# Performance work log

Hardware: AMD Instinct MI355X
Metric: run time of the kernel (lower is better)

## Reference

```python
import jax, jax.numpy as jnp
import numpy as np


def setup_inputs() -> dict:
    key = jax.random.key(0)
    B, D, C, H = 4096, 64, 128, 512
    ks = jax.random.split(key, 6)
    return {
        "q_z_x_params": jax.random.normal(ks[0], (B, C), jnp.float32),
        "eps": jax.random.normal(ks[1], (B, D), jnp.float32),
        "W1": jax.random.normal(ks[2], (D + C, H), jnp.float32) / np.sqrt(D + C).astype(np.float32),
        "b1": jnp.zeros((H,), jnp.float32),
        "W2": jax.random.normal(ks[3], (H, H), jnp.float32) / np.sqrt(H).astype(np.float32),
        "b2": jnp.zeros((H,), jnp.float32),
        "W3": jax.random.normal(ks[4], (H, 2 * D), jnp.float32) / np.sqrt(H).astype(np.float32),
        "b3": jnp.zeros((2 * D,), jnp.float32),
    }


def _made_masks(D, C, H):
    # Standard MADE degrees, natural ordering; context columns fully connected.
    m_in = np.arange(1, D + 1)                      # input degrees 1..D
    m_h = (np.arange(H) % (D - 1)) + 1              # hidden degrees 1..D-1
    M1 = np.concatenate([m_h[None, :] >= m_in[:, None],
                         np.ones((C, H), bool)], axis=0)   # (D+C, H)
    M2 = m_h[None, :] >= m_h[:, None]               # (H, H)
    m_out = np.tile(np.arange(1, D + 1), 2)         # (2D,) mean||prescale
    M3 = m_out[None, :] > m_h[:, None]              # (H, 2D)
    f32 = jnp.float32
    return jnp.asarray(M1, f32), jnp.asarray(M2, f32), jnp.asarray(M3, f32)


def reference(q_z_x_params, eps, W1, b1, W2, b2, W3, b3):
    B, D = eps.shape
    C = q_z_x_params.shape[1]
    H = W2.shape[0]
    M1, M2, M3 = _made_masks(D, C, H)
    mW1, mW2, mW3 = W1 * M1, W2 * M2, W3 * M3

    def made(z):
        x = jnp.concatenate([z, q_z_x_params], axis=1)   # (B, D+C)
        h1 = jax.nn.relu(x @ mW1 + b1)
        h2 = jax.nn.relu(h1 @ mW2 + b2)
        out = h2 @ mW3 + b3                              # (B, 2D)
        return out[:, :D], out[:, D:]

    def step(z, i):
        mean, prescale = made(z)
        mu_i = jnp.take(mean, i, axis=1)                 # (B,)
        scale_i = jax.nn.softplus(jnp.take(prescale, i, axis=1))
        z_i = mu_i + scale_i * jnp.take(eps, i, axis=1)  # reparameterized Normal sample
        z = z.at[:, i].set(z_i)
        return z, None

    z0 = jnp.zeros((B, D), eps.dtype)
    z_sample, _ = jax.lax.scan(step, z0, jnp.arange(D))
    return z_sample
```

## Files before the change

kernel.cpp:

```cpp
#include <hip/hip_runtime.h>
#include <math.h>

#define DD 64
#define CC 128
#define HH 512
#define BATCH 4096

typedef __attribute__((ext_vector_type(2))) float f32x2;

__device__ __forceinline__ f32x2 splat2(float x) { f32x2 v; v[0] = x; v[1] = x; return v; }

__device__ __forceinline__ float fast_softplus(float x) {
    float t = exp2f(-fabsf(x) * 1.44269504f);
    return fmaxf(x, 0.f) + 0.69314718f * log2f(1.f + t);
}

__device__ __forceinline__ float bcast(float x, int l) {
    return __int_as_float(__builtin_amdgcn_readlane(__float_as_int(x), l));
}

typedef const __attribute__((address_space(1))) void* as1_cptr;
typedef __attribute__((address_space(3))) void* as3_ptr;
__device__ __forceinline__ void glds16(const float* g, float* l) {
    __builtin_amdgcn_global_load_lds((as1_cptr)g, (as3_ptr)l, 16, 0, 0);
}

__global__ __launch_bounds__(256, 2) void made_sample(
    const float* __restrict__ ctx,
    const float* __restrict__ eps,
    const float* __restrict__ W1,
    const float* __restrict__ b1,
    const float* __restrict__ W2,
    const float* __restrict__ b2,
    const float* __restrict__ W3,
    const float* __restrict__ b3,
    float* __restrict__ out)
{
    const int lane  = threadIdx.x & 63;
    const int w     = threadIdx.x >> 6;
    const int rbase = blockIdx.x * 8 + w * 2;
    const int jbase = 8 * lane;

    __shared__ float sbuf[2][10 * HH];

    int deg[8];
    #pragma unroll
    for (int u = 0; u < 8; ++u) deg[u] = (jbase + u) % 63 + 1;

    auto load8v = [&](const float* base_, f32x2* r_) {
        float4 a = *(const float4*)(base_ + lane * 4);
        float4 b = *(const float4*)(base_ + 256 + lane * 4);
        r_[0][0] = a.x; r_[0][1] = a.y; r_[1][0] = a.z; r_[1][1] = a.w;
        r_[2][0] = b.x; r_[2][1] = b.y; r_[3][0] = b.z; r_[3][1] = b.w;
    };
    auto stage_row = [&](const float* src, float* dst) {
        glds16(src + lane * 8,     dst);
        glds16(src + lane * 8 + 4, dst + 256);
    };

    f32x2 p1[2][4], p2[2][4], acc[2];
    #pragma unroll
    for (int j = 0; j < 4; ++j) {
        f32x2 t1, t2;
        t1[0] = b1[jbase + 2 * j]; t1[1] = b1[jbase + 2 * j + 1];
        t2[0] = b2[jbase + 2 * j]; t2[1] = b2[jbase + 2 * j + 1];
        p1[0][j] = t1; p1[1][j] = t1;
        p2[0][j] = t2; p2[1][j] = t2;
    }
    acc[0] = splat2(0.f);
    acc[1] = splat2(0.f);

    float ca[2], cb[2], ep[2];
    #pragma unroll
    for (int r = 0; r < 2; ++r) {
        ca[r] = ctx[(rbase + r) * CC + lane];
        cb[r] = ctx[(rbase + r) * CC + 64 + lane];
        ep[r] = eps[(rbase + r) * DD + lane];
    }
    const float b3m = b3[lane];
    const float b3p = b3[64 + lane];

    auto stage_ctx = [&](int ch, float* buf) {
        #pragma unroll
        for (int q2 = 0; q2 < 2; ++q2) {
            const int q = 2 * w + q2;
            stage_row(W1 + (DD + 8 * ch + q) * HH, buf + q * HH);
        }
    };
    auto stage_step = [&](int in, float* buf) {
        const int basen = (in == 0) ? 0 : (in - 1);
        #pragma unroll
        for (int rr = 0; rr < 3; ++rr) {
            const int r = w + 4 * rr;
            if (r <= 9) {
                const float* src;
                if (r < 9) {
                    int k = basen + 63 * r;
                    if (k >= HH) k = HH - 8;
                    src = W2 + k * HH;
                } else {
                    src = W1 + in * HH;
                }
                stage_row(src, buf + r * HH);
            }
        }
    };

    stage_ctx(0, sbuf[0]);
    __syncthreads();
    #pragma unroll 1
    for (int ch = 0; ch < 16; ++ch) {
        float* cur = sbuf[ch & 1];
        float* nxt = sbuf[(ch + 1) & 1];
        if (ch < 15) stage_ctx(ch + 1, nxt);
        else         stage_step(0, sbuf[0]);
        #pragma unroll
        for (int q = 0; q < 8; ++q) {
            f32x2 wv[4];
            load8v(cur + q * HH, wv);
            const int c = 8 * ch + q;
            #pragma unroll
            for (int r = 0; r < 2; ++r) {
                const float cv = bcast((ch < 8) ? ca[r] : cb[r], c & 63);
                const f32x2 cv2 = splat2(cv);
                #pragma unroll
                for (int j = 0; j < 4; ++j) p1[r][j] += cv2 * wv[j];
            }
        }
        __syncthreads();
    }

    float z[2] = {0.f, 0.f};

    #pragma unroll 1
    for (int i = 0; i < DD; ++i) {
        float* cur = sbuf[i & 1];
        float* nxt = sbuf[(i + 1) & 1];
        if (i < 63) stage_step(i + 1, nxt);

        const int base = (i == 0) ? 0 : (i - 1);

        f32x2 w3v[9];
        #pragma unroll
        for (int t = 0; t < 9; ++t) {
            const int k  = base + 63 * t;
            const int ks = (k < HH) ? k : (HH - 1);
            w3v[t][0] = W3[ks * (2 * DD) + lane];
            w3v[t][1] = W3[ks * (2 * DD) + 64 + lane];
        }

        float m[2];
        #pragma unroll
        for (int r = 0; r < 2; ++r) {
            float mv = 0.f;
            #pragma unroll
            for (int u = 0; u < 8; ++u)
                mv = (deg[u] == i) ? p1[r][u >> 1][u & 1] : mv;
            m[r] = fmaxf(mv, 0.f);
        }

        #pragma unroll
        for (int t = 0; t < 9; ++t) {
            const int k = base + 63 * t;
            f32x2 wv[4];
            load8v(cur + t * HH, wv);
            float h0, h1v;
            if (t == 8) {
                const float vm = (k < HH) ? 1.f : 0.f;
                h0  = vm * bcast(m[0], 63);
                h1v = vm * bcast(m[1], 63);
            } else {
                h0  = bcast(m[0], k >> 3);
                h1v = bcast(m[1], k >> 3);
            }
            const f32x2 h0v = splat2(h0), h1vv = splat2(h1v);
            #pragma unroll
            for (int j = 0; j < 4; ++j) {
                p2[0][j] += h0v  * wv[j];
                p2[1][j] += h1vv * wv[j];
            }
        }

        float hn[2];
        #pragma unroll
        for (int r = 0; r < 2; ++r) {
            float hv = 0.f;
            #pragma unroll
            for (int u = 0; u < 8; ++u)
                hv = (deg[u] == i) ? p2[r][u >> 1][u & 1] : hv;
            hn[r] = fmaxf(hv, 0.f);
        }

        #pragma unroll
        for (int t = 0; t < 9; ++t) {
            const int k = base + 63 * t;
            float h0, h1v;
            if (t == 8) {
                const float vm = (k < HH) ? 1.f : 0.f;
                h0  = vm * bcast(hn[0], 63);
                h1v = vm * bcast(hn[1], 63);
            } else {
                h0  = bcast(hn[0], k >> 3);
                h1v = bcast(hn[1], k >> 3);
            }
            acc[0] += splat2(h0)  * w3v[t];
            acc[1] += splat2(h1v) * w3v[t];
        }

        f32x2 w1v[4];
        load8v(cur + 9 * HH, w1v);
        #pragma unroll
        for (int r = 0; r < 2; ++r) {
            const float am = acc[r][0] + b3m;
            const float ap = acc[r][1] + b3p;
            const float sp = fast_softplus(ap);
            const float zc = fmaf(sp, ep[r], am);
            const float zi = bcast(zc, i);
            if (lane == i) z[r] = zi;
            const f32x2 zi2 = splat2(zi);
            #pragma unroll
            for (int j = 0; j < 4; ++j) p1[r][j] += zi2 * w1v[j];
        }

        __syncthreads();
    }

    #pragma unroll
    for (int r = 0; r < 2; ++r) out[(rbase + r) * DD + lane] = z[r];
}

extern "C" void kernel_launch(void* const* d_in, const int* in_sizes, int n_in,
                              void* d_out, int out_size, void* d_ws, size_t ws_size,
                              hipStream_t stream) {
    const float* ctx = (const float*)d_in[0];
    const float* eps = (const float*)d_in[1];
    const float* W1  = (const float*)d_in[2];
    const float* b1  = (const float*)d_in[3];
    const float* W2  = (const float*)d_in[4];
    const float* b2  = (const float*)d_in[5];
    const float* W3  = (const float*)d_in[6];
    const float* b3  = (const float*)d_in[7];
    (void)d_ws; (void)ws_size; (void)in_sizes; (void)n_in; (void)out_size;

    made_sample<<<BATCH / 8, 256, 0, stream>>>(ctx, eps, W1, b1, W2, b2, W3, b3,
                                               (float*)d_out);
}
```

Baseline: 184.7 us.

## Stage W2 and context weights as fp16 and shrink blocks to 128 threads

Adds a pre-kernel that converts W2 and the context rows of W1 to fp16 in the workspace. The main kernel now stages half-width rows into LDS, halving staging traffic and LDS footprint. It also cuts blocks to two waves (4 rows each), doubling the grid. Packed f32x2 FMAs are replaced by scalar fmaf with fp16-to-fp32 converts, and W2 fragments are preloaded into registers. Weight precision drops to fp16, and the extra kernel adds launch overhead.

After: 208.4 us. +12.8%, slower.

```diff
diff --git a/kernel.cpp b/kernel.cpp
--- a/kernel.cpp
+++ b/kernel.cpp
@@ -6,9 +6,14 @@
 #define HH 512
 #define BATCH 4096
 
-typedef __attribute__((ext_vector_type(2))) float f32x2;
-
-__device__ __forceinline__ f32x2 splat2(float x) { f32x2 v; v[0] = x; v[1] = x; return v; }
+typedef _Float16 f16;
+
+__global__ void to_f16(const float* __restrict__ W1, const float* __restrict__ W2,
+                       f16* __restrict__ w2h, f16* __restrict__ w1ch) {
+    int idx = blockIdx.x * 256 + threadIdx.x;
+    if (idx < HH * HH) w2h[idx] = (f16)W2[idx];
+    else               w1ch[idx - HH * HH] = (f16)W1[DD * HH + (idx - HH * HH)];
+}
 
 __device__ __forceinline__ float fast_softplus(float x) {
     float t = exp2f(-fabsf(x) * 1.44269504f);
@@ -21,54 +26,46 @@
 
 typedef const __attribute__((address_space(1))) void* as1_cptr;
 typedef __attribute__((address_space(3))) void* as3_ptr;
-__device__ __forceinline__ void glds16(const float* g, float* l) {
+__device__ __forceinline__ void glds16(const void* g, float* l) {
     __builtin_amdgcn_global_load_lds((as1_cptr)g, (as3_ptr)l, 16, 0, 0);
 }
 
-__global__ __launch_bounds__(256, 2) void made_sample(
+union HW { float4 f4; f16 h[8]; };
+
+#define SLOT_W1 (9 * 256)
+#define BUF_F   (SLOT_W1 + 512)
+
+__global__ __launch_bounds__(128, 2) void made_sample(
     const float* __restrict__ ctx,
     const float* __restrict__ eps,
     const float* __restrict__ W1,
     const float* __restrict__ b1,
-    const float* __restrict__ W2,
     const float* __restrict__ b2,
     const float* __restrict__ W3,
     const float* __restrict__ b3,
+    const f16*   __restrict__ w2h,
+    const f16*   __restrict__ w1ch,
     float* __restrict__ out)
 {
     const int lane  = threadIdx.x & 63;
     const int w     = threadIdx.x >> 6;
-    const int rbase = blockIdx.x * 8 + w * 2;
+    const int rbase = blockIdx.x * 4 + w * 2;
     const int jbase = 8 * lane;
 
-    __shared__ float sbuf[2][10 * HH];
+    __shared__ float sbuf[2][BUF_F];
 
     int deg[8];
     #pragma unroll
     for (int u = 0; u < 8; ++u) deg[u] = (jbase + u) % 63 + 1;
 
-    auto load8v = [&](const float* base_, f32x2* r_) {
-        float4 a = *(const float4*)(base_ + lane * 4);
-        float4 b = *(const float4*)(base_ + 256 + lane * 4);
-        r_[0][0] = a.x; r_[0][1] = a.y; r_[1][0] = a.z; r_[1][1] = a.w;
-        r_[2][0] = b.x; r_[2][1] = b.y; r_[3][0] = b.z; r_[3][1] = b.w;
-    };
-    auto stage_row = [&](const float* src, float* dst) {
-        glds16(src + lane * 8,     dst);
-        glds16(src + lane * 8 + 4, dst + 256);
-    };
-
-    f32x2 p1[2][4], p2[2][4], acc[2];
-    #pragma unroll
-    for (int j = 0; j < 4; ++j) {
-        f32x2 t1, t2;
-        t1[0] = b1[jbase + 2 * j]; t1[1] = b1[jbase + 2 * j + 1];
-        t2[0] = b2[jbase + 2 * j]; t2[1] = b2[jbase + 2 * j + 1];
-        p1[0][j] = t1; p1[1][j] = t1;
-        p2[0][j] = t2; p2[1][j] = t2;
-    }
-    acc[0] = splat2(0.f);
-    acc[1] = splat2(0.f);
+    float p1[2][8], p2[2][8], acc[2][2];
+    #pragma unroll
+    for (int u = 0; u < 8; ++u) {
+        float t1 = b1[jbase + u], t2 = b2[jbase + u];
+        p1[0][u] = t1; p1[1][u] = t1;
+        p2[0][u] = t2; p2[1][u] = t2;
+    }
+    acc[0][0] = 0.f; acc[0][1] = 0.f; acc[1][0] = 0.f; acc[1][1] = 0.f;
 
     float ca[2], cb[2], ep[2];
     #pragma unroll
@@ -82,26 +79,21 @@
 
     auto stage_ctx = [&](int ch, float* buf) {
         #pragma unroll
-        for (int q2 = 0; q2 < 2; ++q2) {
-            const int q = 2 * w + q2;
-            stage_row(W1 + (DD + 8 * ch + q) * HH, buf + q * HH);
-        }
+        for (int q = 0; q < 8; q += 2)
+            glds16(w1ch + (8 * ch + q + w) * HH + lane * 8, buf + (q + w) * 256);
     };
     auto stage_step = [&](int in, float* buf) {
         const int basen = (in == 0) ? 0 : (in - 1);
         #pragma unroll
-        for (int rr = 0; rr < 3; ++rr) {
-            const int r = w + 4 * rr;
-            if (r <= 9) {
-                const float* src;
-                if (r < 9) {
-                    int k = basen + 63 * r;
-                    if (k >= HH) k = HH - 8;
-                    src = W2 + k * HH;
-                } else {
-                    src = W1 + in * HH;
-                }
-                stage_row(src, buf + r * HH);
+        for (int o = w; o < 11; o += 2) {
+            if (o < 9) {
+                int k = basen + 63 * o;
+                if (k >= HH) k = HH - 1;
+                glds16(w2h + k * HH + lane * 8, buf + o * 256);
+            } else if (o == 9) {
+                glds16(W1 + in * HH + lane * 8, buf + SLOT_W1);
+            } else {
+                glds16(W1 + in * HH + lane * 8 + 4, buf + SLOT_W1 + 256);
             }
         }
     };
@@ -116,15 +108,14 @@
         else         stage_step(0, sbuf[0]);
         #pragma unroll
         for (int q = 0; q < 8; ++q) {
-            f32x2 wv[4];
-            load8v(cur + q * HH, wv);
+            HW uw; uw.f4 = *(const float4*)(cur + q * 256 + lane * 4);
             const int c = 8 * ch + q;
             #pragma unroll
             for (int r = 0; r < 2; ++r) {
                 const float cv = bcast((ch < 8) ? ca[r] : cb[r], c & 63);
-                const f32x2 cv2 = splat2(cv);
                 #pragma unroll
-                for (int j = 0; j < 4; ++j) p1[r][j] += cv2 * wv[j];
+                for (int u = 0; u < 8; ++u)
+                    p1[r][u] = fmaf((float)uw.h[u], cv, p1[r][u]);
             }
         }
         __syncthreads();
@@ -140,13 +131,25 @@
 
         const int base = (i == 0) ? 0 : (i - 1);
 
-        f32x2 w3v[9];
+        float w3m[9], w3p[9];
         #pragma unroll
         for (int t = 0; t < 9; ++t) {
             const int k  = base + 63 * t;
             const int ks = (k < HH) ? k : (HH - 1);
-            w3v[t][0] = W3[ks * (2 * DD) + lane];
-            w3v[t][1] = W3[ks * (2 * DD) + 64 + lane];
+            w3m[t] = W3[ks * (2 * DD) + lane];
+            w3p[t] = W3[ks * (2 * DD) + 64 + lane];
+        }
+
+        HW w2v[9];
+        #pragma unroll
+        for (int t = 0; t < 9; ++t)
+            w2v[t].f4 = *(const float4*)(cur + t * 256 + lane * 4);
+        float w1v[8];
+        {
+            float4 a = *(const float4*)(cur + SLOT_W1 + lane * 4);
+            float4 b = *(const float4*)(cur + SLOT_W1 + 256 + lane * 4);
+            w1v[0] = a.x; w1v[1] = a.y; w1v[2] = a.z; w1v[3] = a.w;
+            w1v[4] = b.x; w1v[5] = b.y; w1v[6] = b.z; w1v[7] = b.w;
         }
 
         float m[2];
@@ -154,16 +157,13 @@
         for (int r = 0; r < 2; ++r) {
             float mv = 0.f;
             #pragma unroll
-            for (int u = 0; u < 8; ++u)
-                mv = (deg[u] == i) ? p1[r][u >> 1][u & 1] : mv;
+            for (int u = 0; u < 8; ++u) mv = (deg[u] == i) ? p1[r][u] : mv;
             m[r] = fmaxf(mv, 0.f);
         }
 
         #pragma unroll
         for (int t = 0; t < 9; ++t) {
             const int k = base + 63 * t;
-            f32x2 wv[4];
-            load8v(cur + t * HH, wv);
             float h0, h1v;
             if (t == 8) {
                 const float vm = (k < HH) ? 1.f : 0.f;
@@ -173,11 +173,10 @@
                 h0  = bcast(m[0], k >> 3);
                 h1v = bcast(m[1], k >> 3);
             }
-            const f32x2 h0v = splat2(h0), h1vv = splat2(h1v);
-            #pragma unroll
-            for (int j = 0; j < 4; ++j) {
-                p2[0][j] += h0v  * wv[j];
-                p2[1][j] += h1vv * wv[j];
+            #pragma unroll
+            for (int u = 0; u < 8; ++u) {
+                p2[0][u] = fmaf((float)w2v[t].h[u], h0,  p2[0][u]);
+                p2[1][u] = fmaf((float)w2v[t].h[u], h1v, p2[1][u]);
             }
         }
 
@@ -186,8 +185,7 @@
         for (int r = 0; r < 2; ++r) {
             float hv = 0.f;
             #pragma unroll
-            for (int u = 0; u < 8; ++u)
-                hv = (deg[u] == i) ? p2[r][u >> 1][u & 1] : hv;
+            for (int u = 0; u < 8; ++u) hv = (deg[u] == i) ? p2[r][u] : hv;
             hn[r] = fmaxf(hv, 0.f);
         }
 
@@ -203,12 +201,12 @@
                 h0  = bcast(hn[0], k >> 3);
                 h1v = bcast(hn[1], k >> 3);
             }
-            acc[0] += splat2(h0)  * w3v[t];
-            acc[1] += splat2(h1v) * w3v[t];
-        }
-
-        f32x2 w1v[4];
-        load8v(cur + 9 * HH, w1v);
+            acc[0][0] = fmaf(h0,  w3m[t], acc[0][0]);
+            acc[0][1] = fmaf(h0,  w3p[t], acc[0][1]);
+            acc[1][0] = fmaf(h1v, w3m[t], acc[1][0]);
+            acc[1][1] = fmaf(h1v, w3p[t], acc[1][1]);
+        }
+
         #pragma unroll
         for (int r = 0; r < 2; ++r) {
             const float am = acc[r][0] + b3m;
@@ -217,9 +215,8 @@
             const float zc = fmaf(sp, ep[r], am);
             const float zi = bcast(zc, i);
             if (lane == i) z[r] = zi;
-            const f32x2 zi2 = splat2(zi);
-            #pragma unroll
-            for (int j = 0; j < 4; ++j) p1[r][j] += zi2 * w1v[j];
+            #pragma unroll
+            for (int u = 0; u < 8; ++u) p1[r][u] = fmaf(zi, w1v[u], p1[r][u]);
         }
 
         __syncthreads();
@@ -240,8 +237,11 @@
     const float* b2  = (const float*)d_in[5];
     const float* W3  = (const float*)d_in[6];
     const float* b3  = (const float*)d_in[7];
-    (void)d_ws; (void)ws_size; (void)in_sizes; (void)n_in; (void)out_size;
-
-    made_sample<<<BATCH / 8, 256, 0, stream>>>(ctx, eps, W1, b1, W2, b2, W3, b3,
-                                               (float*)d_out);
-}
+
+    f16* w2h  = (f16*)d_ws;
+    f16* w1ch = w2h + HH * HH;
+
+    to_f16<<<(HH * HH + CC * HH) / 256, 256, 0, stream>>>(W1, W2, w2h, w1ch);
+    made_sample<<<BATCH / 4, 128, 0, stream>>>(ctx, eps, W1, b1, b2, W3, b3,
+                                               w2h, w1ch, (float*)d_out);
+}
```

## Halve block size, skip zero-activation W2 rows, and load W1 rows directly

Applied to the files above, without the earlier changes.

Blocks shrink from 4 to 2 waves and 4 rows each, doubling the grid and reducing the shared buffer to 9 rows. The W1 step row is now loaded straight from global memory into registers instead of being staged through LDS. Staging and the 9th W2/W3 term run only when the index is still in range (i<=8), which removes the masked work. The layer-2 update is skipped when the broadcast hidden activation is zero for both rows, a wave-uniform branch that exploits ReLU sparsity at the cost of extra branching.

Result: slower. 198.0 us (+7.2%).

```diff
diff --git a/kernel.cpp b/kernel.cpp
--- a/kernel.cpp
+++ b/kernel.cpp
@@ -15,8 +15,11 @@
     return fmaxf(x, 0.f) + 0.69314718f * log2f(1.f + t);
 }
 
+__device__ __forceinline__ int bcasti(float x, int l) {
+    return __builtin_amdgcn_readlane(__float_as_int(x), l);
+}
 __device__ __forceinline__ float bcast(float x, int l) {
-    return __int_as_float(__builtin_amdgcn_readlane(__float_as_int(x), l));
+    return __int_as_float(bcasti(x, l));
 }
 
 typedef const __attribute__((address_space(1))) void* as1_cptr;
@@ -25,7 +28,7 @@
     __builtin_amdgcn_global_load_lds((as1_cptr)g, (as3_ptr)l, 16, 0, 0);
 }
 
-__global__ __launch_bounds__(256, 2) void made_sample(
+__global__ __launch_bounds__(128, 2) void made_sample(
     const float* __restrict__ ctx,
     const float* __restrict__ eps,
     const float* __restrict__ W1,
@@ -38,10 +41,10 @@
 {
     const int lane  = threadIdx.x & 63;
     const int w     = threadIdx.x >> 6;
-    const int rbase = blockIdx.x * 8 + w * 2;
+    const int rbase = blockIdx.x * 4 + w * 2;
     const int jbase = 8 * lane;
 
-    __shared__ float sbuf[2][10 * HH];
+    __shared__ float sbuf[2][9 * HH];
 
     int deg[8];
     #pragma unroll
@@ -53,10 +56,6 @@
         r_[0][0] = a.x; r_[0][1] = a.y; r_[1][0] = a.z; r_[1][1] = a.w;
         r_[2][0] = b.x; r_[2][1] = b.y; r_[3][0] = b.z; r_[3][1] = b.w;
     };
-    auto stage_row = [&](const float* src, float* dst) {
-        glds16(src + lane * 8,     dst);
-        glds16(src + lane * 8 + 4, dst + 256);
-    };
 
     f32x2 p1[2][4], p2[2][4], acc[2];
     #pragma unroll
@@ -82,26 +81,23 @@
 
     auto stage_ctx = [&](int ch, float* buf) {
         #pragma unroll
-        for (int q2 = 0; q2 < 2; ++q2) {
-            const int q = 2 * w + q2;
-            stage_row(W1 + (DD + 8 * ch + q) * HH, buf + q * HH);
+        for (int o = 0; o < 8; ++o) {
+            const int oo = 2 * o + w;
+            const int r = oo >> 1, hf = oo & 1;
+            glds16(W1 + (DD + 8 * ch + r) * HH + lane * 8 + hf * 4,
+                   buf + r * HH + hf * 256);
         }
     };
     auto stage_step = [&](int in, float* buf) {
         const int basen = (in == 0) ? 0 : (in - 1);
-        #pragma unroll
-        for (int rr = 0; rr < 3; ++rr) {
-            const int r = w + 4 * rr;
-            if (r <= 9) {
-                const float* src;
-                if (r < 9) {
-                    int k = basen + 63 * r;
-                    if (k >= HH) k = HH - 8;
-                    src = W2 + k * HH;
-                } else {
-                    src = W1 + in * HH;
-                }
-                stage_row(src, buf + r * HH);
+        const int nops = (in <= 8) ? 18 : 16;
+        #pragma unroll
+        for (int o = 0; o < 9; ++o) {
+            const int oo = 2 * o + w;
+            if (oo < nops) {
+                const int r = oo >> 1, hf = oo & 1;
+                glds16(W2 + (basen + 63 * r) * HH + lane * 8 + hf * 4,
+                       buf + r * HH + hf * 256);
             }
         }
     };
@@ -142,11 +138,22 @@
 
         f32x2 w3v[9];
         #pragma unroll
-        for (int t = 0; t < 9; ++t) {
-            const int k  = base + 63 * t;
-            const int ks = (k < HH) ? k : (HH - 1);
-            w3v[t][0] = W3[ks * (2 * DD) + lane];
-            w3v[t][1] = W3[ks * (2 * DD) + 64 + lane];
+        for (int t = 0; t < 8; ++t) {
+            const int k = base + 63 * t;
+            w3v[t][0] = W3[k * (2 * DD) + lane];
+            w3v[t][1] = W3[k * (2 * DD) + 64 + lane];
+        }
+        if (i <= 8) {
+            const int k = base + 504;
+            w3v[8][0] = W3[k * (2 * DD) + lane];
+            w3v[8][1] = W3[k * (2 * DD) + 64 + lane];
+        }
+        f32x2 w1v[4];
+        {
+            float4 a = *(const float4*)(W1 + i * HH + lane * 8);
+            float4 b = *(const float4*)(W1 + i * HH + lane * 8 + 4);
+            w1v[0][0] = a.x; w1v[0][1] = a.y; w1v[1][0] = a.z; w1v[1][1] = a.w;
+            w1v[2][0] = b.x; w1v[2][1] = b.y; w1v[3][0] = b.z; w1v[3][1] = b.w;
         }
 
         float m[2];
@@ -160,24 +167,41 @@
         }
 
         #pragma unroll
-        for (int t = 0; t < 9; ++t) {
+        for (int t = 0; t < 8; ++t) {
             const int k = base + 63 * t;
-            f32x2 wv[4];
-            load8v(cur + t * HH, wv);
-            float h0, h1v;
-            if (t == 8) {
-                const float vm = (k < HH) ? 1.f : 0.f;
-                h0  = vm * bcast(m[0], 63);
-                h1v = vm * bcast(m[1], 63);
-            } else {
-                h0  = bcast(m[0], k >> 3);
-                h1v = bcast(m[1], k >> 3);
-            }
-            const f32x2 h0v = splat2(h0), h1vv = splat2(h1v);
-            #pragma unroll
-            for (int j = 0; j < 4; ++j) {
-                p2[0][j] += h0v  * wv[j];
-                p2[1][j] += h1vv * wv[j];
+            const int hb0 = bcasti(m[0], k >> 3);
+            const int hb1 = bcasti(m[1], k >> 3);
+            if (hb0 | hb1) {
+                f32x2 wv[4];
+                load8v(cur + t * HH, wv);
+                if (hb0) {
+                    const f32x2 h = splat2(__int_as_float(hb0));
+                    #pragma unroll
+                    for (int j = 0; j < 4; ++j) p2[0][j] += h * wv[j];
+                }
+                if (hb1) {
+                    const f32x2 h = splat2(__int_as_float(hb1));
+                    #pragma unroll
+                    for (int j = 0; j < 4; ++j) p2[1][j] += h * wv[j];
+                }
+            }
+        }
+        if (i <= 8) {
+            const int hb0 = bcasti(m[0], 63);
+            const int hb1 = bcasti(m[1], 63);
+            if (hb0 | hb1) {
+                f32x2 wv[4];
+                load8v(cur + 8 * HH, wv);
+                if (hb0) {
+                    const f32x2 h = splat2(__int_as_float(hb0));
+                    #pragma unroll
+                    for (int j = 0; j < 4; ++j) p2[0][j] += h * wv[j];
+                }
+                if (hb1) {
+                    const f32x2 h = splat2(__int_as_float(hb1));
+                    #pragma unroll
+                    for (int j = 0; j < 4; ++j) p2[1][j] += h * wv[j];
+                }
             }
         }
 
@@ -192,23 +216,16 @@
         }
 
         #pragma unroll
-        for (int t = 0; t < 9; ++t) {
+        for (int t = 0; t < 8; ++t) {
             const int k = base + 63 * t;
-            float h0, h1v;
-            if (t == 8) {
-                const float vm = (k < HH) ? 1.f : 0.f;
-                h0  = vm * bcast(hn[0], 63);
-                h1v = vm * bcast(hn[1], 63);
-            } else {
-                h0  = bcast(hn[0], k >> 3);
-                h1v = bcast(hn[1], k >> 3);
-            }
-            acc[0] += splat2(h0)  * w3v[t];
-            acc[1] += splat2(h1v) * w3v[t];
-        }
-
-        f32x2 w1v[4];
-        load8v(cur + 9 * HH, w1v);
+            acc[0] += splat2(bcast(hn[0], k >> 3)) * w3v[t];
+            acc[1] += splat2(bcast(hn[1], k >> 3)) * w3v[t];
+        }
+        if (i <= 8) {
+            acc[0] += splat2(bcast(hn[0], 63)) * w3v[8];
+            acc[1] += splat2(bcast(hn[1], 63)) * w3v[8];
+        }
+
         #pragma unroll
         for (int r = 0; r < 2; ++r) {
             const float am = acc[r][0] + b3m;
@@ -242,6 +259,6 @@
     const float* b3  = (const float*)d_in[7];
     (void)d_ws; (void)ws_size; (void)in_sizes; (void)n_in; (void)out_size;
 
-    made_sample<<<BATCH / 8, 256, 0, stream>>>(ctx, eps, W1, b1, W2, b2, W3, b3,
+    made_sample<<<BATCH / 4, 128, 0, stream>>>(ctx, eps, W1, b1, W2, b2, W3, b3,
                                                (float*)d_out);
 }
```

## Process four rows per wave and stage W3 slices through LDS

Applied to the files above, without the earlier changes.

Each wave now handles four batch rows instead of two, so every LDS weight load is reused across twice as many rows, and the grid is halved to 256 blocks. The per-step W3 rows move from direct global loads into the LDS double buffer, prefetched alongside the W2 and W1 slices with async global-to-LDS copies. The cost is twice as many accumulator registers and launch bounds dropped to one block per CU, which lowers occupancy and leaves fewer blocks than CUs to hide latency.

After: 226.8 us. +22.8%, slower.

```diff
diff --git a/kernel.cpp b/kernel.cpp
--- a/kernel.cpp
+++ b/kernel.cpp
@@ -24,8 +24,15 @@
 __device__ __forceinline__ void glds16(const float* g, float* l) {
     __builtin_amdgcn_global_load_lds((as1_cptr)g, (as3_ptr)l, 16, 0, 0);
 }
-
-__global__ __launch_bounds__(256, 2) void made_sample(
+__device__ __forceinline__ void glds4(const float* g, float* l) {
+    __builtin_amdgcn_global_load_lds((as1_cptr)g, (as3_ptr)l, 4, 0, 0);
+}
+
+#define W1_SLOT 4608
+#define W3_SLOT 5120
+#define BUF_F   6272
+
+__global__ __launch_bounds__(256, 1) void made_sample(
     const float* __restrict__ ctx,
     const float* __restrict__ eps,
     const float* __restrict__ W1,
@@ -38,41 +45,30 @@
 {
     const int lane  = threadIdx.x & 63;
     const int w     = threadIdx.x >> 6;
-    const int rbase = blockIdx.x * 8 + w * 2;
+    const int rbase = blockIdx.x * 16 + w * 4;
     const int jbase = 8 * lane;
 
-    __shared__ float sbuf[2][10 * HH];
+    __shared__ float sbuf[2][BUF_F];
 
     int deg[8];
     #pragma unroll
     for (int u = 0; u < 8; ++u) deg[u] = (jbase + u) % 63 + 1;
 
-    auto load8v = [&](const float* base_, f32x2* r_) {
-        float4 a = *(const float4*)(base_ + lane * 4);
-        float4 b = *(const float4*)(base_ + 256 + lane * 4);
-        r_[0][0] = a.x; r_[0][1] = a.y; r_[1][0] = a.z; r_[1][1] = a.w;
-        r_[2][0] = b.x; r_[2][1] = b.y; r_[3][0] = b.z; r_[3][1] = b.w;
-    };
-    auto stage_row = [&](const float* src, float* dst) {
-        glds16(src + lane * 8,     dst);
-        glds16(src + lane * 8 + 4, dst + 256);
-    };
-
-    f32x2 p1[2][4], p2[2][4], acc[2];
+    f32x2 p1[4][4], p2[4][4], acc[4];
     #pragma unroll
     for (int j = 0; j < 4; ++j) {
         f32x2 t1, t2;
         t1[0] = b1[jbase + 2 * j]; t1[1] = b1[jbase + 2 * j + 1];
         t2[0] = b2[jbase + 2 * j]; t2[1] = b2[jbase + 2 * j + 1];
-        p1[0][j] = t1; p1[1][j] = t1;
-        p2[0][j] = t2; p2[1][j] = t2;
-    }
-    acc[0] = splat2(0.f);
-    acc[1] = splat2(0.f);
-
-    float ca[2], cb[2], ep[2];
-    #pragma unroll
-    for (int r = 0; r < 2; ++r) {
+        #pragma unroll
+        for (int r = 0; r < 4; ++r) { p1[r][j] = t1; p2[r][j] = t2; }
+    }
+    #pragma unroll
+    for (int r = 0; r < 4; ++r) acc[r] = splat2(0.f);
+
+    float ca[4], cb[4], ep[4];
+    #pragma unroll
+    for (int r = 0; r < 4; ++r) {
         ca[r] = ctx[(rbase + r) * CC + lane];
         cb[r] = ctx[(rbase + r) * CC + 64 + lane];
         ep[r] = eps[(rbase + r) * DD + lane];
@@ -82,26 +78,32 @@
 
     auto stage_ctx = [&](int ch, float* buf) {
         #pragma unroll
-        for (int q2 = 0; q2 < 2; ++q2) {
-            const int q = 2 * w + q2;
-            stage_row(W1 + (DD + 8 * ch + q) * HH, buf + q * HH);
+        for (int o4 = 0; o4 < 4; ++o4) {
+            const int o = 4 * o4 + w;
+            const int q = o >> 1, hf = o & 1;
+            glds16(W1 + (DD + 8 * ch + q) * HH + lane * 8 + hf * 4,
+                   buf + q * 512 + hf * 256);
         }
     };
     auto stage_step = [&](int in, float* buf) {
         const int basen = (in == 0) ? 0 : (in - 1);
         #pragma unroll
-        for (int rr = 0; rr < 3; ++rr) {
-            const int r = w + 4 * rr;
-            if (r <= 9) {
-                const float* src;
-                if (r < 9) {
-                    int k = basen + 63 * r;
-                    if (k >= HH) k = HH - 8;
-                    src = W2 + k * HH;
-                } else {
-                    src = W1 + in * HH;
-                }
-                stage_row(src, buf + r * HH);
+        for (int o10 = 0; o10 < 10; ++o10) {
+            const int o = 4 * o10 + w;
+            if (o < 18) {
+                const int t = o >> 1, hf = o & 1;
+                int k = basen + 63 * t;
+                if (k >= HH) k = HH - 1;
+                glds16(W2 + k * HH + lane * 8 + hf * 4, buf + t * 512 + hf * 256);
+            } else if (o < 36) {
+                const int u2 = o - 18, t = u2 >> 1, hf = u2 & 1;
+                int k = basen + 63 * t;
+                if (k >= HH) k = HH - 1;
+                glds4(W3 + k * (2 * DD) + hf * 64 + lane,
+                      buf + W3_SLOT + t * 128 + hf * 64);
+            } else {
+                const int hf = o & 1;
+                glds16(W1 + in * HH + lane * 8 + hf * 4, buf + W1_SLOT + hf * 256);
             }
         }
     };
@@ -111,106 +113,107 @@
     #pragma unroll 1
     for (int ch = 0; ch < 16; ++ch) {
         float* cur = sbuf[ch & 1];
-        float* nxt = sbuf[(ch + 1) & 1];
-        if (ch < 15) stage_ctx(ch + 1, nxt);
+        if (ch < 15) stage_ctx(ch + 1, sbuf[(ch + 1) & 1]);
         else         stage_step(0, sbuf[0]);
         #pragma unroll
         for (int q = 0; q < 8; ++q) {
             f32x2 wv[4];
-            load8v(cur + q * HH, wv);
+            {
+                float4 a = *(const float4*)(cur + q * 512 + lane * 4);
+                float4 b = *(const float4*)(cur + q * 512 + 256 + lane * 4);
+                wv[0][0] = a.x; wv[0][1] = a.y; wv[1][0] = a.z; wv[1][1] = a.w;
+                wv[2][0] = b.x; wv[2][1] = b.y; wv[3][0] = b.z; wv[3][1] = b.w;
+            }
             const int c = 8 * ch + q;
             #pragma unroll
-            for (int r = 0; r < 2; ++r) {
-                const float cv = bcast((ch < 8) ? ca[r] : cb[r], c & 63);
-                const f32x2 cv2 = splat2(cv);
+            for (int r = 0; r < 4; ++r) {
+                const f32x2 cv = splat2(bcast((ch < 8) ? ca[r] : cb[r], c & 63));
                 #pragma unroll
-                for (int j = 0; j < 4; ++j) p1[r][j] += cv2 * wv[j];
+                for (int j = 0; j < 4; ++j) p1[r][j] += cv * wv[j];
             }
         }
         __syncthreads();
     }
 
-    float z[2] = {0.f, 0.f};
+    float z[4] = {0.f, 0.f, 0.f, 0.f};
 
     #pragma unroll 1
     for (int i = 0; i < DD; ++i) {
         float* cur = sbuf[i & 1];
-        float* nxt = sbuf[(i + 1) & 1];
-        if (i < 63) stage_step(i + 1, nxt);
+        if (i < 63) stage_step(i + 1, sbuf[(i + 1) & 1]);
 
         const int base = (i == 0) ? 0 : (i - 1);
-
+        const float vm8 = (i <= 8) ? 1.f : 0.f;
+
+        f32x2 w1v[4];
+        {
+            float4 a = *(const float4*)(cur + W1_SLOT + lane * 4);
+            float4 b = *(const float4*)(cur + W1_SLOT + 256 + lane * 4);
+            w1v[0][0] = a.x; w1v[0][1] = a.y; w1v[1][0] = a.z; w1v[1][1] = a.w;
+            w1v[2][0] = b.x; w1v[2][1] = b.y; w1v[3][0] = b.z; w1v[3][1] = b.w;
+        }
         f32x2 w3v[9];
         #pragma unroll
         for (int t = 0; t < 9; ++t) {
-            const int k  = base + 63 * t;
-            const int ks = (k < HH) ? k : (HH - 1);
-            w3v[t][0] = W3[ks * (2 * DD) + lane];
-            w3v[t][1] = W3[ks * (2 * DD) + 64 + lane];
-        }
-
-        float m[2];
-        #pragma unroll
-        for (int r = 0; r < 2; ++r) {
-            float mv = 0.f;
-            #pragma unroll
-            for (int u = 0; u < 8; ++u)
-                mv = (deg[u] == i) ? p1[r][u >> 1][u & 1] : mv;
-            m[r] = fmaxf(mv, 0.f);
-        }
+            w3v[t][0] = cur[W3_SLOT + t * 128 + lane];
+            w3v[t][1] = cur[W3_SLOT + t * 128 + 64 + lane];
+        }
+
+        float m[4] = {0.f, 0.f, 0.f, 0.f};
+        #pragma unroll
+        for (int u = 0; u < 8; ++u) {
+            const bool hit = (deg[u] == i);
+            #pragma unroll
+            for (int r = 0; r < 4; ++r)
+                m[r] = hit ? p1[r][u >> 1][u & 1] : m[r];
+        }
+        #pragma unroll
+        for (int r = 0; r < 4; ++r) m[r] = fmaxf(m[r], 0.f);
 
         #pragma unroll
         for (int t = 0; t < 9; ++t) {
-            const int k = base + 63 * t;
             f32x2 wv[4];
-            load8v(cur + t * HH, wv);
-            float h0, h1v;
-            if (t == 8) {
-                const float vm = (k < HH) ? 1.f : 0.f;
-                h0  = vm * bcast(m[0], 63);
-                h1v = vm * bcast(m[1], 63);
-            } else {
-                h0  = bcast(m[0], k >> 3);
-                h1v = bcast(m[1], k >> 3);
-            }
-            const f32x2 h0v = splat2(h0), h1vv = splat2(h1v);
-            #pragma unroll
-            for (int j = 0; j < 4; ++j) {
-                p2[0][j] += h0v  * wv[j];
-                p2[1][j] += h1vv * wv[j];
-            }
-        }
-
-        float hn[2];
-        #pragma unroll
-        for (int r = 0; r < 2; ++r) {
-            float hv = 0.f;
-            #pragma unroll
-            for (int u = 0; u < 8; ++u)
-                hv = (deg[u] == i) ? p2[r][u >> 1][u & 1] : hv;
-            hn[r] = fmaxf(hv, 0.f);
-        }
+            {
+                float4 a = *(const float4*)(cur + t * 512 + lane * 4);
+                float4 b = *(const float4*)(cur + t * 512 + 256 + lane * 4);
+                wv[0][0] = a.x; wv[0][1] = a.y; wv[1][0] = a.z; wv[1][1] = a.w;
+                wv[2][0] = b.x; wv[2][1] = b.y; wv[3][0] = b.z; wv[3][1] = b.w;
+            }
+            const int ln = (t == 8) ? 63 : ((base + 63 * t) >> 3);
+            #pragma unroll
+            for (int r = 0; r < 4; ++r) {
+                float h = bcast(m[r], ln);
+                if (t == 8) h *= vm8;
+                const f32x2 hv = splat2(h);
+                #pragma unroll
+                for (int j = 0; j < 4; ++j) p2[r][j] += hv * wv[j];
+            }
+        }
+
+        float hn[4] = {0.f, 0.f, 0.f, 0.f};
+        #pragma unroll
+        for (int u = 0; u < 8; ++u) {
+            const bool hit = (deg[u] == i);
+            #pragma unroll
+            for (int r = 0; r < 4; ++r)
+                hn[r] = hit ? p2[r][u >> 1][u & 1] : hn[r];
+        }
+        #pragma unroll
+        for (int r = 0; r < 4; ++r) hn[r] = fmaxf(hn[r], 0.f);
 
         #pragma unroll
         for (int t = 0; t < 9; ++t) {
-            const int k = base + 63 * t;
-            float h0, h1v;
-            if (t == 8) {
-                const float vm = (k < HH) ? 1.f : 0.f;
-                h0  = vm * bcast(hn[0], 63);
-                h1v = vm * bcast(hn[1], 63);
-            } else {
-                h0  = bcast(hn[0], k >> 3);
-                h1v = bcast(hn[1], k >> 3);
-            }
-            acc[0] += splat2(h0)  * w3v[t];
-            acc[1] += splat2(h1v) * w3v[t];
-        }
-
-        f32x2 w1v[4];
-        load8v(cur + 9 * HH, w1v);
-        #pragma unroll
-        for (int r = 0; r < 2; ++r) {
+            const int ln = (t == 8) ? 63 : ((base + 63 * t) >> 3);
+            #pragma unroll
+            for (int r = 0; r < 4; ++r) {
+                float h = bcast(hn[r], ln);
+                if (t == 8) h *= vm8;
+                acc[r] += splat2(h) * w3v[t];
+            }
+        }
+
+        #pragma unroll
+        for (int r = 0; r < 4; ++r) {
             const float am = acc[r][0] + b3m;
             const float ap = acc[r][1] + b3p;
             const float sp = fast_softplus(ap);
@@ -226,7 +229,7 @@
     }
 
     #pragma unroll
-    for (int r = 0; r < 2; ++r) out[(rbase + r) * DD + lane] = z[r];
+    for (int r = 0; r < 4; ++r) out[(rbase + r) * DD + lane] = z[r];
 }
 
 extern "C" void kernel_launch(void* const* d_in, const int* in_sizes, int n_in,
@@ -242,6 +245,6 @@
     const float* b3  = (const float*)d_in[7];
     (void)d_ws; (void)ws_size; (void)in_sizes; (void)n_in; (void)out_size;
 
-    made_sample<<<BATCH / 8, 256, 0, stream>>>(ctx, eps, W1, b1, W2, b2, W3, b3,
-                                               (float*)d_out);
-}
+    made_sample<<<BATCH / 16, 256, 0, stream>>>(ctx, eps, W1, b1, W2, b2, W3, b3,
+                                                (float*)d_out);
+}
```
